# Optimization experiments

Hardware: AMD Instinct MI355X
Metric: run time of the kernel (lower is better)

The kernel has to match this reference:

```python
import jax, jax.numpy as jnp
import numpy as np

N_NODES = 50000
N_EDGES = 800000
IN_CH = 128
HID = 32
HEADS = 8
OUT_CH = 40
NEG_SLOPE = 0.2


def setup_inputs() -> dict:
    key = jax.random.key(0)
    ks = jax.random.split(key, 12)
    g = lambda k, shape, fan: (jax.random.normal(k, shape, jnp.float32) / np.sqrt(fan).astype(np.float32))
    return {
        "x": jax.random.normal(ks[0], (N_NODES, IN_CH), jnp.float32),
        "edge_index": jax.random.randint(ks[1], (2, N_EDGES), 0, N_NODES, jnp.int64),
        "W1l": g(ks[2], (IN_CH, HEADS * HID), IN_CH),
        "W1r": g(ks[3], (IN_CH, HEADS * HID), IN_CH),
        "att1": g(ks[4], (HEADS, HID), HID),
        "b1": jnp.zeros((HEADS * HID,), jnp.float32),
        "W2l": g(ks[5], (HEADS * HID, HID), HEADS * HID),
        "W2r": g(ks[6], (HEADS * HID, HID), HEADS * HID),
        "att2": g(ks[7], (1, HID), HID),
        "b2": jnp.zeros((HID,), jnp.float32),
        "Wc": g(ks[8], (HID + IN_CH, OUT_CH), HID + IN_CH),
        "bc": jnp.zeros((OUT_CH,), jnp.float32),
    }


def _gatv2(x, ei, Wl, Wr, att, b, heads, ch):
    # GATv2Conv (concat=True): e_ij = att . LeakyReLU(Wl x_j + Wr x_i)
    n = x.shape[0]
    src, dst = ei[0], ei[1]  # message flows src(j) -> dst(i)
    xl = (x @ Wl).reshape(n, heads, ch)  # source transform
    xr = (x @ Wr).reshape(n, heads, ch)  # target transform
    e = jax.nn.leaky_relu(xl[src] + xr[dst], NEG_SLOPE)  # [E, H, C]
    score = jnp.einsum("ehc,hc->eh", e, att)             # [E, H]
    # per-target-node segment softmax (stable)
    m = jax.ops.segment_max(score, dst, num_segments=n)
    alpha = jnp.exp(score - m[dst])
    denom = jax.ops.segment_sum(alpha, dst, num_segments=n)
    alpha = alpha / denom[dst]
    out = jax.ops.segment_sum(alpha[:, :, None] * xl[src], dst, num_segments=n)
    return out.reshape(n, heads * ch) + b


def reference(x, edge_index, W1l, W1r, att1, b1, W2l, W2r, att2, b2, Wc, bc):
    n = x.shape[0]
    ar = jnp.arange(n, dtype=edge_index.dtype)
    ei = jnp.concatenate([edge_index, jnp.stack([ar, ar])], axis=1)  # add self-loops
    h1 = jax.nn.elu(_gatv2(x, ei, W1l, W1r, att1, b1, HEADS, HID))
    h2 = jax.nn.elu(_gatv2(h1, ei, W2l, W2r, att2, b2, 1, HID))
    combined = jnp.concatenate([h2, x], axis=1)
    return combined @ Wc + bc
```

## Files before the change

### kernel.cpp

```cpp
#include <hip/hip_runtime.h>
#include <cstdint>
#include <cstddef>
#include <math.h>

#define NN 50000
#define INCH 128
#define HIDC 32
#define NHEAD 8
#define OUTC 40

typedef unsigned short ushort_t;
using bf16x8 = __attribute__((ext_vector_type(8))) short;
using f32x4  = __attribute__((ext_vector_type(4))) float;

__device__ __forceinline__ float bf2f(unsigned short h) {
    return __uint_as_float(((unsigned int)h) << 16);
}
__device__ __forceinline__ unsigned short f2bf(float f) {
    unsigned int u = __float_as_uint(f);
    u = u + 0x7FFFu + ((u >> 16) & 1u);
    return (unsigned short)(u >> 16);
}


__global__ __launch_bounds__(256) void convert_x(const float* __restrict__ x,
                                                 ushort_t* __restrict__ xb, int total8) {
    int i = blockIdx.x * 256 + threadIdx.x;
    if (i >= total8) return;
    float4 f0 = *(const float4*)(x + (size_t)i * 8);
    float4 f1 = *(const float4*)(x + (size_t)i * 8 + 4);
    ushort4 u0, u1;
    u0.x = f2bf(f0.x); u0.y = f2bf(f0.y); u0.z = f2bf(f0.z); u0.w = f2bf(f0.w);
    u1.x = f2bf(f1.x); u1.y = f2bf(f1.y); u1.z = f2bf(f1.z); u1.w = f2bf(f1.w);
    *(ushort4*)(xb + (size_t)i * 8) = u0;
    *(ushort4*)(xb + (size_t)i * 8 + 4) = u1;
}

__global__ __launch_bounds__(256) void prep_weights(
    const float* __restrict__ W1l, const float* __restrict__ W1r,
    const float* __restrict__ W2l, const float* __restrict__ W2r,
    const float* __restrict__ Wc,
    ushort_t* __restrict__ BT1, ushort_t* __restrict__ BT2, ushort_t* __restrict__ BTc) {
    int b = blockIdx.x, k = threadIdx.x;
    if (b < 512) {
        if (k < 128) {
            float v = (b < 256) ? W1l[(size_t)k * 256 + b] : W1r[(size_t)k * 256 + (b - 256)];
            BT1[(size_t)b * 128 + k] = f2bf(v);
        }
    } else if (b < 576) {
        int c = b - 512;
        float v = (c < 32) ? W2l[(size_t)k * 32 + c] : W2r[(size_t)k * 32 + (c - 32)];
        BT2[(size_t)c * 256 + k] = f2bf(v);
    } else {
        int c = b - 576;
        if (k < 160) BTc[(size_t)c * 160 + k] = f2bf(Wc[(size_t)k * 40 + c]);
    }
}


__global__ void zero_i32(int* p, int n) {
    int i = blockIdx.x * blockDim.x + threadIdx.x;
    if (i < n) p[i] = 0;
}

__global__ void count_deg(const int* __restrict__ ei, int E, int n, int* __restrict__ deg) {
    int e = blockIdx.x * blockDim.x + threadIdx.x;
    if (e >= E + n) return;
    int dst = (e < E) ? ei[E + e] : (e - E);
    atomicAdd(&deg[dst], 1);
}

__global__ __launch_bounds__(1024) void partial_scan(
    const int* __restrict__ deg, int* __restrict__ row_start,
    int* __restrict__ block_total, int n) {
    __shared__ int wsum[16];
    const int tid = threadIdx.x, lane = tid & 63, wid = tid >> 6;
    int i = blockIdx.x * 1024 + tid;
    int v = (i < n) ? deg[i] : 0;
    int s = v;
    #pragma unroll
    for (int off = 1; off < 64; off <<= 1) {
        int t = __shfl_up(s, off, 64);
        if (lane >= off) s += t;
    }
    if (lane == 63) wsum[wid] = s;
    __syncthreads();
    if (wid == 0) {
        int ws = (lane < 16) ? wsum[lane] : 0;
        #pragma unroll
        for (int off = 1; off < 16; off <<= 1) {
            int t = __shfl_up(ws, off, 64);
            if (lane >= off) ws += t;
        }
        if (lane < 16) wsum[lane] = ws;
    }
    __syncthreads();
    int wexcl = wid ? wsum[wid - 1] : 0;
    if (i < n) row_start[i] = wexcl + s - v;
    if (tid == 0) block_total[blockIdx.x] = wsum[15];
}

__global__ void totals_scan(const int* __restrict__ block_total, int* __restrict__ block_off,
                            int* __restrict__ row_start_n, int nb) {
    int j = threadIdx.x;
    int v = (j < nb) ? block_total[j] : 0;
    int s = v;
    #pragma unroll
    for (int off = 1; off < 64; off <<= 1) {
        int t = __shfl_up(s, off, 64);
        if (j >= off) s += t;
    }
    if (j < nb) block_off[j] = s - v;
    if (j == nb - 1) *row_start_n = s;
}

__global__ __launch_bounds__(1024) void add_off(int* __restrict__ row_start, int* __restrict__ cursor,
                                                const int* __restrict__ block_off, int n) {
    int i = blockIdx.x * 1024 + threadIdx.x;
    if (i >= n) return;
    int val = row_start[i] + block_off[blockIdx.x];
    row_start[i] = val;
    cursor[i] = val;
}

__global__ void scatter_edges(const int* __restrict__ ei, int E, int n,
                              int* __restrict__ cursor, int* __restrict__ csr_src) {
    int e = blockIdx.x * blockDim.x + threadIdx.x;
    if (e >= E + n) return;
    int src, dst;
    if (e < E) { src = ei[e]; dst = ei[E + e]; } else { src = dst = e - E; }
    int pos = atomicAdd(&cursor[dst], 1);
    csr_src[pos] = src;
}

__global__ __launch_bounds__(256) void gemm1_mfma(
    const ushort_t* __restrict__ xb, const ushort_t* __restrict__ BT1,
    ushort_t* __restrict__ xlr1, int M) {
    __shared__ ushort_t As[128][72];
    __shared__ ushort_t Bs[128][72];
    const int tid = threadIdx.x;
    const int rowBase = blockIdx.y * 128;
    const int c0 = blockIdx.x * 128;
    const int wid = tid >> 6, lane = tid & 63;
    const int wr = wid >> 1, wc = wid & 1;
    const int l15 = lane & 15, l4 = lane >> 4;
    f32x4 acc[4][4];
    #pragma unroll
    for (int i = 0; i < 4; ++i)
        #pragma unroll
        for (int j = 0; j < 4; ++j)
            #pragma unroll
            for (int q = 0; q < 4; ++q) acc[i][j][q] = 0.f;

    for (int c = 0; c < 2; ++c) {
        #pragma unroll
        for (int h = 0; h < 4; ++h) {
            int idx = h * 256 + tid;
            int r = idx >> 3, seg = idx & 7;
            int row = rowBase + r;
            uint4 v = {0, 0, 0, 0};
            if (row < M) v = *(const uint4*)(xb + (size_t)row * 128 + c * 64 + seg * 8);
            *(uint4*)&As[r][seg * 8] = v;
            *(uint4*)&Bs[r][seg * 8] = *(const uint4*)(BT1 + (size_t)(c0 + r) * 128 + c * 64 + seg * 8);
        }
        __syncthreads();
        #pragma unroll
        for (int kk = 0; kk < 2; ++kk) {
            bf16x8 a[4], b[4];
            #pragma unroll
            for (int f = 0; f < 4; ++f) {
                a[f] = *(const bf16x8*)&As[wr * 64 + f * 16 + l15][kk * 32 + l4 * 8];
                b[f] = *(const bf16x8*)&Bs[wc * 64 + f * 16 + l15][kk * 32 + l4 * 8];
            }
            #pragma unroll
            for (int i = 0; i < 4; ++i)
                #pragma unroll
                for (int j = 0; j < 4; ++j)
                    acc[i][j] = __builtin_amdgcn_mfma_f32_16x16x32_bf16(a[i], b[j], acc[i][j], 0, 0, 0);
        }
        __syncthreads();
    }
    #pragma unroll
    for (int i = 0; i < 4; ++i)
        #pragma unroll
        for (int r = 0; r < 4; ++r) {
            int row = rowBase + wr * 64 + i * 16 + l4 * 4 + r;
            if (row >= M) continue;
            #pragma unroll
            for (int j = 0; j < 4; ++j) {
                int col = c0 + wc * 64 + j * 16 + l15;
                xlr1[(size_t)row * 512 + col] = f2bf(acc[i][j][r]);
            }
        }
}

__global__ __launch_bounds__(256) void gemm2_mfma(
    const ushort_t* __restrict__ h1, const ushort_t* __restrict__ BT2,
    ushort_t* __restrict__ xlr2, int M) {
    __shared__ ushort_t As[128][72];
    __shared__ ushort_t Bs[64][264];
    const int tid = threadIdx.x;
    const int rowBase = blockIdx.x * 128;
    const int wid = tid >> 6, lane = tid & 63;
    const int l15 = lane & 15, l4 = lane >> 4;
    #pragma unroll
    for (int h = 0; h < 8; ++h) {
        int idx = h * 256 + tid;
        int r = idx >> 5, seg = idx & 31;
        *(uint4*)&Bs[r][seg * 8] = *(const uint4*)(BT2 + (size_t)r * 256 + seg * 8);
    }
    f32x4 acc[2][4];
    #pragma unroll
    for (int i = 0; i < 2; ++i)
        #pragma unroll
        for (int j = 0; j < 4; ++j)
            #pragma unroll
            for (int q = 0; q < 4; ++q) acc[i][j][q] = 0.f;

    for (int c = 0; c < 4; ++c) {
        #pragma unroll
        for (int h = 0; h < 4; ++h) {
            int idx = h * 256 + tid;
            int r = idx >> 3, seg = idx & 7;
            int row = rowBase + r;
            uint4 v = {0, 0, 0, 0};
            if (row < M) v = *(const uint4*)(h1 + (size_t)row * 256 + c * 64 + seg * 8);
            *(uint4*)&As[r][seg * 8] = v;
        }
        __syncthreads();
        #pragma unroll
        for (int kk = 0; kk < 2; ++kk) {
            bf16x8 a[2], b[4];
            #pragma unroll
            for (int f = 0; f < 2; ++f)
                a[f] = *(const bf16x8*)&As[wid * 32 + f * 16 + l15][kk * 32 + l4 * 8];
            #pragma unroll
            for (int f = 0; f < 4; ++f)
                b[f] = *(const bf16x8*)&Bs[f * 16 + l15][c * 64 + kk * 32 + l4 * 8];
            #pragma unroll
            for (int i = 0; i < 2; ++i)
                #pragma unroll
                for (int j = 0; j < 4; ++j)
                    acc[i][j] = __builtin_amdgcn_mfma_f32_16x16x32_bf16(a[i], b[j], acc[i][j], 0, 0, 0);
        }
        __syncthreads();
    }
    #pragma unroll
    for (int i = 0; i < 2; ++i)
        #pragma unroll
        for (int r = 0; r < 4; ++r) {
            int row = rowBase + wid * 32 + i * 16 + l4 * 4 + r;
            if (row >= M) continue;
            #pragma unroll
            for (int j = 0; j < 4; ++j) {
                int col = j * 16 + l15;
                xlr2[(size_t)row * 64 + col] = f2bf(acc[i][j][r]);
            }
        }
}

__global__ __launch_bounds__(256) void final_mfma(
    const ushort_t* __restrict__ h2, const ushort_t* __restrict__ xb,
    const ushort_t* __restrict__ BTc, const float* __restrict__ bc,
    float* __restrict__ out, int M) {
    __shared__ ushort_t As[128][168];
    __shared__ ushort_t Bs[48][168];
    const int tid = threadIdx.x;
    const int rowBase = blockIdx.x * 128;
    const int wid = tid >> 6, lane = tid & 63;
    const int l15 = lane & 15, l4 = lane >> 4;
    #pragma unroll
    for (int h = 0; h < 4; ++h) {
        int idx = h * 256 + tid;
        if (idx < 960) {
            int r = idx / 20, seg = idx % 20;
            uint4 v = {0, 0, 0, 0};
            if (r < 40) v = *(const uint4*)(BTc + (size_t)r * 160 + seg * 8);
            *(uint4*)&Bs[r][seg * 8] = v;
        }
    }
    #pragma unroll
    for (int h = 0; h < 10; ++h) {
        int idx = h * 256 + tid;
        int r = idx / 20, seg = idx % 20;
        int row = rowBase + r;
        uint4 v = {0, 0, 0, 0};
        if (row < M)
            v = (seg < 4) ? *(const uint4*)(h2 + (size_t)row * 32 + seg * 8)
                          : *(const uint4*)(xb + (size_t)row * 128 + (seg - 4) * 8);
        *(uint4*)&As[r][seg * 8] = v;
    }
    __syncthreads();
    f32x4 acc[2][3];
    #pragma unroll
    for (int i = 0; i < 2; ++i)
        #pragma unroll
        for (int j = 0; j < 3; ++j)
            #pragma unroll
            for (int q = 0; q < 4; ++q) acc[i][j][q] = 0.f;
    #pragma unroll
    for (int kk = 0; kk < 5; ++kk) {
        bf16x8 a[2], b[3];
        #pragma unroll
        for (int f = 0; f < 2; ++f)
            a[f] = *(const bf16x8*)&As[wid * 32 + f * 16 + l15][kk * 32 + l4 * 8];
        #pragma unroll
        for (int f = 0; f < 3; ++f)
            b[f] = *(const bf16x8*)&Bs[f * 16 + l15][kk * 32 + l4 * 8];
        #pragma unroll
        for (int i = 0; i < 2; ++i)
            #pragma unroll
            for (int j = 0; j < 3; ++j)
                acc[i][j] = __builtin_amdgcn_mfma_f32_16x16x32_bf16(a[i], b[j], acc[i][j], 0, 0, 0);
    }
    #pragma unroll
    for (int i = 0; i < 2; ++i)
        #pragma unroll
        for (int r = 0; r < 4; ++r) {
            int row = rowBase + wid * 32 + i * 16 + l4 * 4 + r;
            if (row >= M) continue;
            #pragma unroll
            for (int j = 0; j < 3; ++j) {
                int col = j * 16 + l15;
                if (col < 40) out[(size_t)row * 40 + col] = acc[i][j][r] + bc[col];
            }
        }
}

__global__ __launch_bounds__(256) void gat_agg1(
    const ushort_t* __restrict__ xlr, const float* __restrict__ att, const float* __restrict__ b,
    const int* __restrict__ row_start, const int* __restrict__ csr_src,
    ushort_t* __restrict__ h1) {
    const int lane = threadIdx.x & 63;
    const int i = blockIdx.x * 4 + (threadIdx.x >> 6);
    const ushort4 xru = *(const ushort4*)(xlr + (size_t)i * 512 + 256 + lane * 4);
    const float xr0 = bf2f(xru.x), xr1 = bf2f(xru.y), xr2 = bf2f(xru.z), xr3 = bf2f(xru.w);
    const float4 at4 = *(const float4*)(att + lane * 4);
    const int p0 = row_start[i], p1 = row_start[i + 1];
    float m = -INFINITY, d = 0.f;
    float a0 = 0.f, a1 = 0.f, a2 = 0.f, a3 = 0.f;
    ushort4 u = *(const ushort4*)(xlr + (size_t)csr_src[p0] * 512 + lane * 4);
    for (int p = p0; p < p1; ++p) {
        float v0 = bf2f(u.x), v1 = bf2f(u.y), v2 = bf2f(u.z), v3 = bf2f(u.w);
        if (p + 1 < p1)
            u = *(const ushort4*)(xlr + (size_t)csr_src[p + 1] * 512 + lane * 4);
        float e0 = v0 + xr0; e0 = fmaxf(e0, 0.f) + 0.2f * fminf(e0, 0.f);
        float e1 = v1 + xr1; e1 = fmaxf(e1, 0.f) + 0.2f * fminf(e1, 0.f);
        float e2 = v2 + xr2; e2 = fmaxf(e2, 0.f) + 0.2f * fminf(e2, 0.f);
        float e3 = v3 + xr3; e3 = fmaxf(e3, 0.f) + 0.2f * fminf(e3, 0.f);
        float sc = e0 * at4.x;
        sc = fmaf(e1, at4.y, sc);
        sc = fmaf(e2, at4.z, sc);
        sc = fmaf(e3, at4.w, sc);
        sc += __shfl_xor(sc, 1);
        sc += __shfl_xor(sc, 2);
        sc += __shfl_xor(sc, 4);
        float mn = fmaxf(m, sc);
        float corr = __expf(m - mn);
        float w = __expf(sc - mn);
        d = d * corr + w;
        a0 = a0 * corr + w * v0;
        a1 = a1 * corr + w * v1;
        a2 = a2 * corr + w * v2;
        a3 = a3 * corr + w * v3;
        m = mn;
    }
    const float4 bb = *(const float4*)(b + lane * 4);
    float inv = 1.f / d;
    float o0 = a0 * inv + bb.x, o1 = a1 * inv + bb.y;
    float o2 = a2 * inv + bb.z, o3 = a3 * inv + bb.w;
    o0 = o0 > 0.f ? o0 : __expf(o0) - 1.f;
    o1 = o1 > 0.f ? o1 : __expf(o1) - 1.f;
    o2 = o2 > 0.f ? o2 : __expf(o2) - 1.f;
    o3 = o3 > 0.f ? o3 : __expf(o3) - 1.f;
    ushort4 ou;
    ou.x = f2bf(o0); ou.y = f2bf(o1); ou.z = f2bf(o2); ou.w = f2bf(o3);
    *(ushort4*)(h1 + (size_t)i * 256 + lane * 4) = ou;
}

__global__ __launch_bounds__(256) void gat_agg2(
    const ushort_t* __restrict__ xlr, const float* __restrict__ att, const float* __restrict__ b,
    const int* __restrict__ row_start, const int* __restrict__ csr_src,
    ushort_t* __restrict__ h2) {
    const int sub = threadIdx.x & 15;
    const int i = blockIdx.x * 16 + (threadIdx.x >> 4);
    const ushort2 xru = *(const ushort2*)(xlr + (size_t)i * 64 + 32 + sub * 2);
    const float xr0 = bf2f(xru.x), xr1 = bf2f(xru.y);
    const float2 atv = *(const float2*)(att + sub * 2);
    const int p0 = row_start[i], p1 = row_start[i + 1];
    float m = -INFINITY, d = 0.f, a0 = 0.f, a1 = 0.f;
    ushort2 u = *(const ushort2*)(xlr + (size_t)csr_src[p0] * 64 + sub * 2);
    for (int p = p0; p < p1; ++p) {
        float v0 = bf2f(u.x), v1 = bf2f(u.y);
        if (p + 1 < p1)
            u = *(const ushort2*)(xlr + (size_t)csr_src[p + 1] * 64 + sub * 2);
        float e0 = v0 + xr0; e0 = fmaxf(e0, 0.f) + 0.2f * fminf(e0, 0.f);
        float e1 = v1 + xr1; e1 = fmaxf(e1, 0.f) + 0.2f * fminf(e1, 0.f);
        float sc = fmaf(e1, atv.y, e0 * atv.x);
        sc += __shfl_xor(sc, 1);
        sc += __shfl_xor(sc, 2);
        sc += __shfl_xor(sc, 4);
        sc += __shfl_xor(sc, 8);
        float mn = fmaxf(m, sc);
        float corr = __expf(m - mn);
        float w = __expf(sc - mn);
        d = d * corr + w;
        a0 = a0 * corr + w * v0;
        a1 = a1 * corr + w * v1;
        m = mn;
    }
    float inv = 1.f / d;
    float o0 = a0 * inv + b[sub * 2];
    float o1 = a1 * inv + b[sub * 2 + 1];
    o0 = o0 > 0.f ? o0 : __expf(o0) - 1.f;
    o1 = o1 > 0.f ? o1 : __expf(o1) - 1.f;
    ushort2 ou; ou.x = f2bf(o0); ou.y = f2bf(o1);
    *(ushort2*)(h2 + (size_t)i * 32 + sub * 2) = ou;
}


extern "C" void kernel_launch(void* const* d_in, const int* in_sizes, int n_in,
                              void* d_out, int out_size, void* d_ws, size_t ws_size,
                              hipStream_t stream) {
    const float* x    = (const float*)d_in[0];
    const int*   ei   = (const int*)d_in[1];
    const float* W1l  = (const float*)d_in[2];
    const float* W1r  = (const float*)d_in[3];
    const float* att1 = (const float*)d_in[4];
    const float* b1   = (const float*)d_in[5];
    const float* W2l  = (const float*)d_in[6];
    const float* W2r  = (const float*)d_in[7];
    const float* att2 = (const float*)d_in[8];
    const float* b2   = (const float*)d_in[9];
    const float* Wc   = (const float*)d_in[10];
    const float* bc   = (const float*)d_in[11];
    float* out = (float*)d_out;

    const int n  = NN;
    const int E  = in_sizes[1] / 2;
    const int TE = E + n;
    const int NB = (n + 1023) / 1024;

    char* ws = (char*)d_ws;
    size_t off = 0;
    auto alloc = [&](size_t bytes) { void* p = ws + off; off += (bytes + 255) & ~(size_t)255; return p; };
    ushort_t* xb   = (ushort_t*)alloc((size_t)n * 128 * 2);
    ushort_t* xlr1 = (ushort_t*)alloc((size_t)n * 512 * 2);
    ushort_t* h1   = (ushort_t*)alloc((size_t)n * 256 * 2);
    ushort_t* xlr2 = (ushort_t*)alloc((size_t)n * 64 * 2);
    ushort_t* h2   = (ushort_t*)alloc((size_t)n * 32 * 2);
    ushort_t* BT1  = (ushort_t*)alloc(512 * 128 * 2);
    ushort_t* BT2  = (ushort_t*)alloc(64 * 256 * 2);
    ushort_t* BTc  = (ushort_t*)alloc(40 * 160 * 2);
    int* row_start   = (int*)alloc((size_t)(n + 1) * 4);
    int* cursor      = (int*)alloc((size_t)(n + 1) * 4);
    int* deg         = (int*)alloc((size_t)n * 4);
    int* block_total = (int*)alloc((size_t)NB * 4);
    int* block_off   = (int*)alloc((size_t)NB * 4);
    int* csr_src     = (int*)alloc((size_t)TE * 4);

    convert_x<<<(n * 128 / 8 + 255) / 256, 256, 0, stream>>>(x, xb, n * 128 / 8);
    prep_weights<<<616, 256, 0, stream>>>(W1l, W1r, W2l, W2r, Wc, BT1, BT2, BTc);

    zero_i32<<<(n + 255) / 256, 256, 0, stream>>>(deg, n);
    count_deg<<<(TE + 255) / 256, 256, 0, stream>>>(ei, E, n, deg);
    partial_scan<<<NB, 1024, 0, stream>>>(deg, row_start, block_total, n);
    totals_scan<<<1, 64, 0, stream>>>(block_total, block_off, row_start + n, NB);
    add_off<<<NB, 1024, 0, stream>>>(row_start, cursor, block_off, n);
    scatter_edges<<<(TE + 255) / 256, 256, 0, stream>>>(ei, E, n, cursor, csr_src);

    gemm1_mfma<<<dim3(4, (n + 127) / 128), 256, 0, stream>>>(xb, BT1, xlr1, n);
    gat_agg1<<<n / 4, 256, 0, stream>>>(xlr1, att1, b1, row_start, csr_src, h1);

    gemm2_mfma<<<(n + 127) / 128, 256, 0, stream>>>(h1, BT2, xlr2, n);
    gat_agg2<<<n / 16, 256, 0, stream>>>(xlr2, att2, b2, row_start, csr_src, h2);

    final_mfma<<<(n + 127) / 128, 256, 0, stream>>>(h2, xb, BTc, bc, out, n);
}
```

Measured before the change: 368.6 us.

## Split LeakyReLU into linear+abs terms, drop online max, parallelize layer-2 edges

LeakyReLU is rewritten as 0.6*e + 0.4*|e|, so the linear part of the attention score becomes per-node dot products. New dots1 and dots2 kernels precompute these, and the aggregation loops only add the abs term. The online-softmax running max and its correction exponentials are removed, so scores are exponentiated directly, which risks overflow when scores are large. gat_agg2 now processes four edges per wave in parallel and reduces at the end. Preprocessing kernels are merged into one launch, and the degree buffer is zeroed with hipMemsetAsync.

```diff
diff --git a/kernel.cpp b/kernel.cpp
--- a/kernel.cpp
+++ b/kernel.cpp
@@ -22,53 +22,48 @@
     return (unsigned short)(u >> 16);
 }
 
-
-__global__ __launch_bounds__(256) void convert_x(const float* __restrict__ x,
-                                                 ushort_t* __restrict__ xb, int total8) {
-    int i = blockIdx.x * 256 + threadIdx.x;
-    if (i >= total8) return;
-    float4 f0 = *(const float4*)(x + (size_t)i * 8);
-    float4 f1 = *(const float4*)(x + (size_t)i * 8 + 4);
-    ushort4 u0, u1;
-    u0.x = f2bf(f0.x); u0.y = f2bf(f0.y); u0.z = f2bf(f0.z); u0.w = f2bf(f0.w);
-    u1.x = f2bf(f1.x); u1.y = f2bf(f1.y); u1.z = f2bf(f1.z); u1.w = f2bf(f1.w);
-    *(ushort4*)(xb + (size_t)i * 8) = u0;
-    *(ushort4*)(xb + (size_t)i * 8 + 4) = u1;
-}
-
-__global__ __launch_bounds__(256) void prep_weights(
+__global__ __launch_bounds__(256) void prep_all(
+    const float* __restrict__ x, ushort_t* __restrict__ xb, int total8,
     const float* __restrict__ W1l, const float* __restrict__ W1r,
     const float* __restrict__ W2l, const float* __restrict__ W2r,
     const float* __restrict__ Wc,
-    ushort_t* __restrict__ BT1, ushort_t* __restrict__ BT2, ushort_t* __restrict__ BTc) {
-    int b = blockIdx.x, k = threadIdx.x;
-    if (b < 512) {
-        if (k < 128) {
-            float v = (b < 256) ? W1l[(size_t)k * 256 + b] : W1r[(size_t)k * 256 + (b - 256)];
-            BT1[(size_t)b * 128 + k] = f2bf(v);
-        }
-    } else if (b < 576) {
-        int c = b - 512;
-        float v = (c < 32) ? W2l[(size_t)k * 32 + c] : W2r[(size_t)k * 32 + (c - 32)];
-        BT2[(size_t)c * 256 + k] = f2bf(v);
+    ushort_t* __restrict__ BT1, ushort_t* __restrict__ BT2, ushort_t* __restrict__ BTc,
+    const int* __restrict__ ei, int E, int n, int* __restrict__ deg, int CX) {
+    const int blk = blockIdx.x;
+    const int tid = threadIdx.x;
+    if (blk < CX) {
+        int i = blk * 256 + tid;
+        if (i >= total8) return;
+        float4 f0 = *(const float4*)(x + (size_t)i * 8);
+        float4 f1 = *(const float4*)(x + (size_t)i * 8 + 4);
+        ushort4 u0, u1;
+        u0.x = f2bf(f0.x); u0.y = f2bf(f0.y); u0.z = f2bf(f0.z); u0.w = f2bf(f0.w);
+        u1.x = f2bf(f1.x); u1.y = f2bf(f1.y); u1.z = f2bf(f1.z); u1.w = f2bf(f1.w);
+        *(ushort4*)(xb + (size_t)i * 8) = u0;
+        *(ushort4*)(xb + (size_t)i * 8 + 4) = u1;
+    } else if (blk < CX + 616) {
+        int b = blk - CX, k = tid;
+        if (b < 512) {
+            if (k < 128) {
+                float v = (b < 256) ? W1l[(size_t)k * 256 + b] : W1r[(size_t)k * 256 + (b - 256)];
+                BT1[(size_t)b * 128 + k] = f2bf(v);
+            }
+        } else if (b < 576) {
+            int c = b - 512;
+            float v = (c < 32) ? W2l[(size_t)k * 32 + c] : W2r[(size_t)k * 32 + (c - 32)];
+            BT2[(size_t)c * 256 + k] = f2bf(v);
+        } else {
+            int c = b - 576;
+            if (k < 160) BTc[(size_t)c * 160 + k] = f2bf(Wc[(size_t)k * 40 + c]);
+        }
     } else {
-        int c = b - 576;
-        if (k < 160) BTc[(size_t)c * 160 + k] = f2bf(Wc[(size_t)k * 40 + c]);
-    }
-}
-
-
-__global__ void zero_i32(int* p, int n) {
-    int i = blockIdx.x * blockDim.x + threadIdx.x;
-    if (i < n) p[i] = 0;
-}
-
-__global__ void count_deg(const int* __restrict__ ei, int E, int n, int* __restrict__ deg) {
-    int e = blockIdx.x * blockDim.x + threadIdx.x;
-    if (e >= E + n) return;
-    int dst = (e < E) ? ei[E + e] : (e - E);
-    atomicAdd(&deg[dst], 1);
-}
+        int e = (blk - CX - 616) * 256 + tid;
+        if (e >= E + n) return;
+        int dst = (e < E) ? ei[E + e] : (e - E);
+        atomicAdd(&deg[dst], 1);
+    }
+}
+
 
 __global__ __launch_bounds__(1024) void partial_scan(
     const int* __restrict__ deg, int* __restrict__ row_start,
@@ -194,6 +189,87 @@
         }
 }
 
+__global__ __launch_bounds__(256) void dots1(
+    const ushort_t* __restrict__ xlr, const float* __restrict__ att,
+    float* __restrict__ dl, float* __restrict__ dr) {
+    const int lane = threadIdx.x & 63;
+    const int i = blockIdx.x * 4 + (threadIdx.x >> 6);
+    const int l31 = lane & 31;
+    const float4 atA = *(const float4*)(att + l31 * 8);
+    const float4 atB = *(const float4*)(att + l31 * 8 + 4);
+    ushort4 ua = *(const ushort4*)(xlr + (size_t)i * 512 + lane * 8);
+    ushort4 ub = *(const ushort4*)(xlr + (size_t)i * 512 + lane * 8 + 4);
+    float q = atA.x * bf2f(ua.x);
+    q = fmaf(atA.y, bf2f(ua.y), q);
+    q = fmaf(atA.z, bf2f(ua.z), q);
+    q = fmaf(atA.w, bf2f(ua.w), q);
+    q = fmaf(atB.x, bf2f(ub.x), q);
+    q = fmaf(atB.y, bf2f(ub.y), q);
+    q = fmaf(atB.z, bf2f(ub.z), q);
+    q = fmaf(atB.w, bf2f(ub.w), q);
+    q += __shfl_xor(q, 1);
+    q += __shfl_xor(q, 2);
+    if ((lane & 3) == 0) {
+        int head = l31 >> 2;
+        if (lane < 32) dl[(size_t)i * 8 + head] = q;
+        else           dr[(size_t)i * 8 + head] = q;
+    }
+}
+
+__global__ __launch_bounds__(256) void gat_agg1(
+    const ushort_t* __restrict__ xlr, const float* __restrict__ dl,
+    const float* __restrict__ dr, const float* __restrict__ att,
+    const float* __restrict__ b,
+    const int* __restrict__ row_start, const int* __restrict__ csr_src,
+    ushort_t* __restrict__ h1) {
+    const int lane = threadIdx.x & 63;
+    const int i = blockIdx.x * 4 + (threadIdx.x >> 6);
+    const int head = lane >> 3;
+    const ushort4 xru = *(const ushort4*)(xlr + (size_t)i * 512 + 256 + lane * 4);
+    const float xr0 = bf2f(xru.x), xr1v = bf2f(xru.y), xr2v = bf2f(xru.z), xr3v = bf2f(xru.w);
+    const float4 at4 = *(const float4*)(att + lane * 4);
+    const float cbase = 0.6f * dr[(size_t)i * 8 + head];
+    const int p0 = row_start[i], p1 = row_start[i + 1];
+    float d = 0.f, a0 = 0.f, a1 = 0.f, a2 = 0.f, a3 = 0.f;
+    int j = csr_src[p0];
+    ushort4 u = *(const ushort4*)(xlr + (size_t)j * 512 + lane * 4);
+    float dlj = dl[(size_t)j * 8 + head];
+    for (int p = p0; p < p1; ++p) {
+        float v0 = bf2f(u.x), v1 = bf2f(u.y), v2 = bf2f(u.z), v3 = bf2f(u.w);
+        float base = fmaf(0.6f, dlj, cbase);
+        if (p + 1 < p1) {
+            int jn = csr_src[p + 1];
+            u = *(const ushort4*)(xlr + (size_t)jn * 512 + lane * 4);
+            dlj = dl[(size_t)jn * 8 + head];
+        }
+        float e0 = v0 + xr0, e1 = v1 + xr1v, e2 = v2 + xr2v, e3 = v3 + xr3v;
+        float q = at4.x * fabsf(e0);
+        q = fmaf(at4.y, fabsf(e1), q);
+        q = fmaf(at4.z, fabsf(e2), q);
+        q = fmaf(at4.w, fabsf(e3), q);
+        q += __shfl_xor(q, 1);
+        q += __shfl_xor(q, 2);
+        q += __shfl_xor(q, 4);
+        float w = __expf(fmaf(0.4f, q, base));
+        d += w;
+        a0 = fmaf(w, v0, a0);
+        a1 = fmaf(w, v1, a1);
+        a2 = fmaf(w, v2, a2);
+        a3 = fmaf(w, v3, a3);
+    }
+    const float4 bb = *(const float4*)(b + lane * 4);
+    float inv = 1.f / d;
+    float o0 = fmaf(a0, inv, bb.x), o1 = fmaf(a1, inv, bb.y);
+    float o2 = fmaf(a2, inv, bb.z), o3 = fmaf(a3, inv, bb.w);
+    o0 = o0 > 0.f ? o0 : __expf(o0) - 1.f;
+    o1 = o1 > 0.f ? o1 : __expf(o1) - 1.f;
+    o2 = o2 > 0.f ? o2 : __expf(o2) - 1.f;
+    o3 = o3 > 0.f ? o3 : __expf(o3) - 1.f;
+    ushort4 ou;
+    ou.x = f2bf(o0); ou.y = f2bf(o1); ou.z = f2bf(o2); ou.w = f2bf(o3);
+    *(ushort4*)(h1 + (size_t)i * 256 + lane * 4) = ou;
+}
+
 __global__ __launch_bounds__(256) void gemm2_mfma(
     const ushort_t* __restrict__ h1, const ushort_t* __restrict__ BT2,
     ushort_t* __restrict__ xlr2, int M) {
@@ -257,6 +333,76 @@
                 xlr2[(size_t)row * 64 + col] = f2bf(acc[i][j][r]);
             }
         }
+}
+
+__global__ __launch_bounds__(256) void dots2(
+    const ushort_t* __restrict__ xlr, const float* __restrict__ att,
+    float* __restrict__ dl, float* __restrict__ dr) {
+    const int lane = threadIdx.x & 63;
+    const int i = blockIdx.x * 8 + (threadIdx.x >> 6) * 2 + (lane >> 5);
+    const int sub = lane & 31;
+    const float2 at = *(const float2*)(att + (sub & 15) * 2);
+    ushort2 u = *(const ushort2*)(xlr + (size_t)i * 64 + sub * 2);
+    float q = at.x * bf2f(u.x);
+    q = fmaf(at.y, bf2f(u.y), q);
+    q += __shfl_xor(q, 1);
+    q += __shfl_xor(q, 2);
+    q += __shfl_xor(q, 4);
+    q += __shfl_xor(q, 8);
+    if ((sub & 15) == 0) {
+        if (sub < 16) dl[i] = q;
+        else          dr[i] = q;
+    }
+}
+
+__global__ __launch_bounds__(256) void gat_agg2(
+    const ushort_t* __restrict__ xlr, const float* __restrict__ dl,
+    const float* __restrict__ dr, const float* __restrict__ att,
+    const float* __restrict__ b,
+    const int* __restrict__ row_start, const int* __restrict__ csr_src,
+    ushort_t* __restrict__ h2) {
+    const int lane = threadIdx.x & 63;
+    const int i = blockIdx.x * 4 + (threadIdx.x >> 6);
+    const int g = lane >> 4, h = lane & 15;
+    const ushort2 xru = *(const ushort2*)(xlr + (size_t)i * 64 + 32 + h * 2);
+    const float xr0 = bf2f(xru.x), xr1v = bf2f(xru.y);
+    const float2 atv = *(const float2*)(att + h * 2);
+    const float cbase = 0.6f * dr[i];
+    const int p0 = row_start[i], p1 = row_start[i + 1];
+    float d = 0.f, a0 = 0.f, a1 = 0.f;
+    for (int p = p0; p < p1; p += 4) {
+        int pe = p + g;
+        bool val = pe < p1;
+        int pc = val ? pe : p1 - 1;
+        int j = csr_src[pc];
+        ushort2 u = *(const ushort2*)(xlr + (size_t)j * 64 + h * 2);
+        float dlj = dl[j];
+        float v0 = bf2f(u.x), v1 = bf2f(u.y);
+        float e0 = v0 + xr0, e1 = v1 + xr1v;
+        float q = atv.x * fabsf(e0);
+        q = fmaf(atv.y, fabsf(e1), q);
+        q += __shfl_xor(q, 1);
+        q += __shfl_xor(q, 2);
+        q += __shfl_xor(q, 4);
+        q += __shfl_xor(q, 8);
+        float sc = fmaf(0.4f, q, fmaf(0.6f, dlj, cbase));
+        float w = val ? __expf(sc) : 0.f;
+        d += w;
+        a0 = fmaf(w, v0, a0);
+        a1 = fmaf(w, v1, a1);
+    }
+    d += __shfl_xor(d, 16);  d += __shfl_xor(d, 32);
+    a0 += __shfl_xor(a0, 16); a0 += __shfl_xor(a0, 32);
+    a1 += __shfl_xor(a1, 16); a1 += __shfl_xor(a1, 32);
+    if (g == 0) {
+        float inv = 1.f / d;
+        float o0 = fmaf(a0, inv, b[h * 2]);
+        float o1 = fmaf(a1, inv, b[h * 2 + 1]);
+        o0 = o0 > 0.f ? o0 : __expf(o0) - 1.f;
+        o1 = o1 > 0.f ? o1 : __expf(o1) - 1.f;
+        ushort2 ou; ou.x = f2bf(o0); ou.y = f2bf(o1);
+        *(ushort2*)(h2 + (size_t)i * 32 + h * 2) = ou;
+    }
 }
 
 __global__ __launch_bounds__(256) void final_mfma(
@@ -325,97 +471,6 @@
                 if (col < 40) out[(size_t)row * 40 + col] = acc[i][j][r] + bc[col];
             }
         }
-}
-
-__global__ __launch_bounds__(256) void gat_agg1(
-    const ushort_t* __restrict__ xlr, const float* __restrict__ att, const float* __restrict__ b,
-    const int* __restrict__ row_start, const int* __restrict__ csr_src,
-    ushort_t* __restrict__ h1) {
-    const int lane = threadIdx.x & 63;
-    const int i = blockIdx.x * 4 + (threadIdx.x >> 6);
-    const ushort4 xru = *(const ushort4*)(xlr + (size_t)i * 512 + 256 + lane * 4);
-    const float xr0 = bf2f(xru.x), xr1 = bf2f(xru.y), xr2 = bf2f(xru.z), xr3 = bf2f(xru.w);
-    const float4 at4 = *(const float4*)(att + lane * 4);
-    const int p0 = row_start[i], p1 = row_start[i + 1];
-    float m = -INFINITY, d = 0.f;
-    float a0 = 0.f, a1 = 0.f, a2 = 0.f, a3 = 0.f;
-    ushort4 u = *(const ushort4*)(xlr + (size_t)csr_src[p0] * 512 + lane * 4);
-    for (int p = p0; p < p1; ++p) {
-        float v0 = bf2f(u.x), v1 = bf2f(u.y), v2 = bf2f(u.z), v3 = bf2f(u.w);
-        if (p + 1 < p1)
-            u = *(const ushort4*)(xlr + (size_t)csr_src[p + 1] * 512 + lane * 4);
-        float e0 = v0 + xr0; e0 = fmaxf(e0, 0.f) + 0.2f * fminf(e0, 0.f);
-        float e1 = v1 + xr1; e1 = fmaxf(e1, 0.f) + 0.2f * fminf(e1, 0.f);
-        float e2 = v2 + xr2; e2 = fmaxf(e2, 0.f) + 0.2f * fminf(e2, 0.f);
-        float e3 = v3 + xr3; e3 = fmaxf(e3, 0.f) + 0.2f * fminf(e3, 0.f);
-        float sc = e0 * at4.x;
-        sc = fmaf(e1, at4.y, sc);
-        sc = fmaf(e2, at4.z, sc);
-        sc = fmaf(e3, at4.w, sc);
-        sc += __shfl_xor(sc, 1);
-        sc += __shfl_xor(sc, 2);
-        sc += __shfl_xor(sc, 4);
-        float mn = fmaxf(m, sc);
-        float corr = __expf(m - mn);
-        float w = __expf(sc - mn);
-        d = d * corr + w;
-        a0 = a0 * corr + w * v0;
-        a1 = a1 * corr + w * v1;
-        a2 = a2 * corr + w * v2;
-        a3 = a3 * corr + w * v3;
-        m = mn;
-    }
-    const float4 bb = *(const float4*)(b + lane * 4);
-    float inv = 1.f / d;
-    float o0 = a0 * inv + bb.x, o1 = a1 * inv + bb.y;
-    float o2 = a2 * inv + bb.z, o3 = a3 * inv + bb.w;
-    o0 = o0 > 0.f ? o0 : __expf(o0) - 1.f;
-    o1 = o1 > 0.f ? o1 : __expf(o1) - 1.f;
-    o2 = o2 > 0.f ? o2 : __expf(o2) - 1.f;
-    o3 = o3 > 0.f ? o3 : __expf(o3) - 1.f;
-    ushort4 ou;
-    ou.x = f2bf(o0); ou.y = f2bf(o1); ou.z = f2bf(o2); ou.w = f2bf(o3);
-    *(ushort4*)(h1 + (size_t)i * 256 + lane * 4) = ou;
-}
-
-__global__ __launch_bounds__(256) void gat_agg2(
-    const ushort_t* __restrict__ xlr, const float* __restrict__ att, const float* __restrict__ b,
-    const int* __restrict__ row_start, const int* __restrict__ csr_src,
-    ushort_t* __restrict__ h2) {
-    const int sub = threadIdx.x & 15;
-    const int i = blockIdx.x * 16 + (threadIdx.x >> 4);
-    const ushort2 xru = *(const ushort2*)(xlr + (size_t)i * 64 + 32 + sub * 2);
-    const float xr0 = bf2f(xru.x), xr1 = bf2f(xru.y);
-    const float2 atv = *(const float2*)(att + sub * 2);
-    const int p0 = row_start[i], p1 = row_start[i + 1];
-    float m = -INFINITY, d = 0.f, a0 = 0.f, a1 = 0.f;
-    ushort2 u = *(const ushort2*)(xlr + (size_t)csr_src[p0] * 64 + sub * 2);
-    for (int p = p0; p < p1; ++p) {
-        float v0 = bf2f(u.x), v1 = bf2f(u.y);
-        if (p + 1 < p1)
-            u = *(const ushort2*)(xlr + (size_t)csr_src[p + 1] * 64 + sub * 2);
-        float e0 = v0 + xr0; e0 = fmaxf(e0, 0.f) + 0.2f * fminf(e0, 0.f);
-        float e1 = v1 + xr1; e1 = fmaxf(e1, 0.f) + 0.2f * fminf(e1, 0.f);
-        float sc = fmaf(e1, atv.y, e0 * atv.x);
-        sc += __shfl_xor(sc, 1);
-        sc += __shfl_xor(sc, 2);
-        sc += __shfl_xor(sc, 4);
-        sc += __shfl_xor(sc, 8);
-        float mn = fmaxf(m, sc);
-        float corr = __expf(m - mn);
-        float w = __expf(sc - mn);
-        d = d * corr + w;
-        a0 = a0 * corr + w * v0;
-        a1 = a1 * corr + w * v1;
-        m = mn;
-    }
-    float inv = 1.f / d;
-    float o0 = a0 * inv + b[sub * 2];
-    float o1 = a1 * inv + b[sub * 2 + 1];
-    o0 = o0 > 0.f ? o0 : __expf(o0) - 1.f;
-    o1 = o1 > 0.f ? o1 : __expf(o1) - 1.f;
-    ushort2 ou; ou.x = f2bf(o0); ou.y = f2bf(o1);
-    *(ushort2*)(h2 + (size_t)i * 32 + sub * 2) = ou;
 }
 
 
@@ -440,6 +495,8 @@
     const int E  = in_sizes[1] / 2;
     const int TE = E + n;
     const int NB = (n + 1023) / 1024;
+    const int CX = (n * 128 / 8 + 255) / 256;
+    const int CD = (TE + 255) / 256;
 
     char* ws = (char*)d_ws;
     size_t off = 0;
@@ -452,6 +509,10 @@
     ushort_t* BT1  = (ushort_t*)alloc(512 * 128 * 2);
     ushort_t* BT2  = (ushort_t*)alloc(64 * 256 * 2);
     ushort_t* BTc  = (ushort_t*)alloc(40 * 160 * 2);
+    float* dl1 = (float*)alloc((size_t)n * 8 * 4);
+    float* dr1 = (float*)alloc((size_t)n * 8 * 4);
+    float* dl2 = (float*)alloc((size_t)n * 4);
+    float* dr2 = (float*)alloc((size_t)n * 4);
     int* row_start   = (int*)alloc((size_t)(n + 1) * 4);
     int* cursor      = (int*)alloc((size_t)(n + 1) * 4);
     int* deg         = (int*)alloc((size_t)n * 4);
@@ -459,21 +520,22 @@
     int* block_off   = (int*)alloc((size_t)NB * 4);
     int* csr_src     = (int*)alloc((size_t)TE * 4);
 
-    convert_x<<<(n * 128 / 8 + 255) / 256, 256, 0, stream>>>(x, xb, n * 128 / 8);
-    prep_weights<<<616, 256, 0, stream>>>(W1l, W1r, W2l, W2r, Wc, BT1, BT2, BTc);
-
-    zero_i32<<<(n + 255) / 256, 256, 0, stream>>>(deg, n);
-    count_deg<<<(TE + 255) / 256, 256, 0, stream>>>(ei, E, n, deg);
+    hipMemsetAsync(deg, 0, (size_t)n * 4, stream);
+    prep_all<<<CX + 616 + CD, 256, 0, stream>>>(x, xb, n * 128 / 8,
+        W1l, W1r, W2l, W2r, Wc, BT1, BT2, BTc, ei, E, n, deg, CX);
+
     partial_scan<<<NB, 1024, 0, stream>>>(deg, row_start, block_total, n);
     totals_scan<<<1, 64, 0, stream>>>(block_total, block_off, row_start + n, NB);
     add_off<<<NB, 1024, 0, stream>>>(row_start, cursor, block_off, n);
-    scatter_edges<<<(TE + 255) / 256, 256, 0, stream>>>(ei, E, n, cursor, csr_src);
+    scatter_edges<<<CD, 256, 0, stream>>>(ei, E, n, cursor, csr_src);
 
     gemm1_mfma<<<dim3(4, (n + 127) / 128), 256, 0, stream>>>(xb, BT1, xlr1, n);
-    gat_agg1<<<n / 4, 256, 0, stream>>>(xlr1, att1, b1, row_start, csr_src, h1);
+    dots1<<<n / 4, 256, 0, stream>>>(xlr1, att1, dl1, dr1);
+    gat_agg1<<<n / 4, 256, 0, stream>>>(xlr1, dl1, dr1, att1, b1, row_start, csr_src, h1);
 
     gemm2_mfma<<<(n + 127) / 128, 256, 0, stream>>>(h1, BT2, xlr2, n);
-    gat_agg2<<<n / 16, 256, 0, stream>>>(xlr2, att2, b2, row_start, csr_src, h2);
+    dots2<<<n / 8, 256, 0, stream>>>(xlr2, att2, dl2, dr2);
+    gat_agg2<<<n / 4, 256, 0, stream>>>(xlr2, dl2, dr2, att2, b2, row_start, csr_src, h2);
 
     final_mfma<<<(n + 127) / 128, 256, 0, stream>>>(h2, xb, BTc, bc, out, n);
 }
```

Measured after the change: 387.2 us. +5.0%, slower.
